# Kernel tuning notes

Measured on AMD Instinct MI355X. Metric: run time of the kernel, lower is better.

## Reference

```python
import jax, jax.numpy as jnp
import numpy as np

B, T, H, I, O, L = 8, 8192, 256, 256, 256, 2


def setup_inputs() -> dict:
    key = jax.random.key(0)
    ks = jax.random.split(key, 12)
    s = 1.0 / np.sqrt(H)
    inp = {
        "emb": jax.random.normal(ks[0], (B, T, I), jnp.float32),
        "start": jax.random.randint(ks[1], (B, T), 0, 2) > 0,  # bool reset flags
        "h0": jnp.zeros((L, B, H), jnp.float32),               # per-layer initial carry
        "min_w": jax.random.normal(ks[2], (H, I), jnp.float32) * s,
        "min_b": jnp.zeros((H,), jnp.float32),
        "mout_w": jax.random.normal(ks[3], (O, H), jnp.float32) * s,
        "mout_b": jnp.zeros((O,), jnp.float32),
        "Wf_w": jax.random.normal(ks[4], (L, H, H), jnp.float32) * s,
        "Wf_b": jnp.zeros((L, H), jnp.float32),
        "Wh_w": jax.random.normal(ks[5], (L, H, H), jnp.float32) * s,
        "Wh_b": jnp.zeros((L, H), jnp.float32),
        "Uf_w": jax.random.normal(ks[6], (L, H, H), jnp.float32) * s,
        "Uh_w": jax.random.normal(ks[7], (L, H, H), jnp.float32) * s,
        "ff_w": jax.random.normal(ks[8], (L, H, H), jnp.float32) * s,
        "ff_b": jnp.zeros((L, H), jnp.float32),
    }
    return inp


def reference(emb, start, h0, min_w, min_b, mout_w, mout_b,
              Wf_w, Wf_b, Wh_w, Wh_b, Uf_w, Uh_w, ff_w, ff_b):
    # map_in: [B,T,I] -> [B,T,H]
    x = jnp.einsum('bti,hi->bth', emb, min_w) + min_b
    start_t = start.T  # [T,B]
    h_final = []
    for l in range(L):
        # Precompute input-side projections outside the scan (time-parallel).
        xf = jnp.einsum('bth,oh->bto', x, Wf_w[l]) + Wf_b[l]  # [B,T,H]
        xh = jnp.einsum('bth,oh->bto', x, Wh_w[l]) + Wh_b[l]  # [B,T,H]
        Uf = Uf_w[l]
        Uh = Uh_w[l]

        def step(h, inp):
            xft, xht, st = inp  # [B,H], [B,H], [B]
            # Resettable: zero the carry where a new episode starts.
            h = jnp.where(st[:, None], jnp.zeros_like(h), h)
            f = jax.nn.sigmoid(xft + h @ Uf.T)
            h_hat = jnp.tanh(xht + (f * h) @ Uh.T)
            h_new = (1.0 - f) * h + f * h_hat
            return h_new, h_new

        hT, z = jax.lax.scan(step, h0[l],
                             (xf.transpose(1, 0, 2), xh.transpose(1, 0, 2), start_t))
        h_final.append(hT)
        z = z.transpose(1, 0, 2)  # [B,T,H]
        # per-layer feedforward + leaky_relu (slope 0.01)
        x = jax.nn.leaky_relu(jnp.einsum('bth,oh->bto', z, ff_w[l]) + ff_b[l])
    out = jnp.einsum('bth,oh->bto', x, mout_w) + mout_b  # [B,T,O]
    return out, jnp.stack(h_final)  # ([B,T,O], [L,B,H])
```

## Files before the change

kernel.cpp:

```cpp
#include <hip/hip_runtime.h>
#include <hip/hip_fp16.h>
#include <cstdint>
#include <cstddef>

#define BATCH 8
#define TT 8192
#define HD 256
#define RTOT (BATCH * TT)
#define HC 16
#define NPAIR (TT / (2 * HC))
#define MSTR 272

typedef __attribute__((ext_vector_type(4))) float    f32x4;
typedef __attribute__((ext_vector_type(8))) _Float16 f16x8;
typedef __attribute__((ext_vector_type(4))) _Float16 f16x4;

typedef __attribute__((address_space(1))) const void gvoid_t;
typedef __attribute__((address_space(3))) void lvoid_t;

__device__ __forceinline__ void gl_lds16(const void* g, void* l) {
  __builtin_amdgcn_global_load_lds((gvoid_t*)g, (lvoid_t*)l, 16, 0, 0);
}

__device__ __forceinline__ void ldsbar() {
  asm volatile("s_waitcnt lgkmcnt(0)" ::: "memory");
  __builtin_amdgcn_s_barrier();
  __builtin_amdgcn_sched_barrier(0x7F);
}

__device__ __forceinline__ void gbar() {
  __builtin_amdgcn_s_barrier();
  __builtin_amdgcn_sched_barrier(0);
  asm volatile("" ::: "memory");
}

__global__ void detect_start_par(const unsigned int* __restrict__ s,
                                 int* __restrict__ bad) {
  const unsigned int w = s[blockIdx.x * blockDim.x + threadIdx.x];
  const unsigned int b0 = w & 255u, b1 = (w >> 8) & 255u,
                     b2 = (w >> 16) & 255u, b3 = (w >> 24) & 255u;
  const int bi = (b1 | b2 | b3) != 0;
  const int bf = (b0 != 0) || (b1 != 0) ||
                 (b2 != 0 && b2 != 0x80u) || (b3 != 0 && b3 != 0x3fu);
  if (__any(bi) && (threadIdx.x & 63) == 0) atomicOr(&bad[0], 1);
  if (__any(bf) && (threadIdx.x & 63) == 0) atomicOr(&bad[1], 1);
}

__global__ void conv_f16(const float* __restrict__ in, _Float16* __restrict__ out,
                         const int n) {
  const int i = (blockIdx.x * blockDim.x + threadIdx.x) * 8;
  if (i + 7 >= n) return;
  const float4 a = *(const float4*)&in[i];
  const float4 b = *(const float4*)&in[i + 4];
  f16x8 v;
  v[0] = (_Float16)a.x; v[1] = (_Float16)a.y; v[2] = (_Float16)a.z; v[3] = (_Float16)a.w;
  v[4] = (_Float16)b.x; v[5] = (_Float16)b.y; v[6] = (_Float16)b.z; v[7] = (_Float16)b.w;
  *(f16x8*)&out[i] = v;
}

__global__ void conv_w8(const float* p0, const float* p1, const float* p2,
                        const float* p3, const float* p4, const float* p5,
                        const float* p6, const float* p7,
                        _Float16* __restrict__ out) {
  const int seg = blockIdx.y;
  const float* p;
  switch (seg) {
    case 0: p = p0; break; case 1: p = p1; break;
    case 2: p = p2; break; case 3: p = p3; break;
    case 4: p = p4; break; case 5: p = p5; break;
    case 6: p = p6; break; default: p = p7; break;
  }
  const int i = (blockIdx.x * blockDim.x + threadIdx.x) * 8;
  const float4 a = *(const float4*)&p[i];
  const float4 b = *(const float4*)&p[i + 4];
  f16x8 v;
  v[0] = (_Float16)a.x; v[1] = (_Float16)a.y; v[2] = (_Float16)a.z; v[3] = (_Float16)a.w;
  v[4] = (_Float16)b.x; v[5] = (_Float16)b.y; v[6] = (_Float16)b.z; v[7] = (_Float16)b.w;
  *(f16x8*)&out[(size_t)seg * 65536 + i] = v;
}

__global__ void swz_w(const float* __restrict__ Uf, const float* __restrict__ Uh,
                      _Float16* __restrict__ outp) {
  const int gid  = blockIdx.x * 256 + threadIdx.x;
  const int lane = gid & 63;
  const int w    = (gid >> 6) & 7;
  const int f    = (gid >> 9) & 15;
  const int mat  = (gid >> 13) & 1;
  const int l    = gid >> 14;
  const int fr = lane & 15, fq = lane >> 4;
  const int tile = f >> 3, kc = f & 7;
  const int nrow = (w * 2 + tile) * 16 + fr;
  const int kb   = kc * 32 + fq * 8;
  const float* src = (mat ? Uh : Uf) + (size_t)l * 65536 + nrow * 256 + kb;
  const float4 a = *(const float4*)src;
  const float4 b = *(const float4*)(src + 4);
  f16x8 v;
  v[0] = (_Float16)a.x; v[1] = (_Float16)a.y; v[2] = (_Float16)a.z; v[3] = (_Float16)a.w;
  v[4] = (_Float16)b.x; v[5] = (_Float16)b.y; v[6] = (_Float16)b.z; v[7] = (_Float16)b.w;
  *(f16x8*)&outp[(size_t)gid * 8] = v;
}

__global__ __launch_bounds__(256, 2) void gemm_fused(
    const _Float16* __restrict__ A,
    const _Float16* __restrict__ W1, const float* __restrict__ b1, const int act1,
    const _Float16* __restrict__ Wa, const float* __restrict__ ba,
    const _Float16* __restrict__ Wb, const float* __restrict__ bb,
    _Float16* __restrict__ Ca, _Float16* __restrict__ Cb,
    float* __restrict__ C32) {
  __shared__ __align__(16) char smem[59392];
  _Float16* mid = (_Float16*)smem;
  char* stg = smem + 34816;
  _Float16* EP = (_Float16*)stg;

  const int tid  = threadIdx.x;
  const int wave = tid >> 6, lane = tid & 63;
  const int wm = wave >> 1, wn = wave & 1;
  const int bm = blockIdx.x * 64;
  const int lrow  = tid >> 2;
  const int lcol8 = (tid & 3) * 8;
  const int fr = lane & 15;
  const int fq = lane >> 4;

  for (int nh = 0; nh < 2; nh++) {
    f32x4 acc[2][4];
#pragma unroll
    for (int i = 0; i < 2; i++)
#pragma unroll
      for (int j = 0; j < 4; j++) acc[i][j] = (f32x4){0.f, 0.f, 0.f, 0.f};
    float bv[4];
#pragma unroll
    for (int ni = 0; ni < 4; ni++)
      bv[ni] = b1[nh * 128 + wn * 64 + ni * 16 + fr];

    auto STA = [&](int kk, int bb2) {
      const int k0 = kk * 32;
      gl_lds16(&A[(size_t)(bm + lrow) * HD + k0 + lcol8],
               stg + bb2 * 12288 + wave * 1024);
#pragma unroll
      for (int is = 0; is < 2; is++)
        gl_lds16(&W1[(size_t)(nh * 128 + is * 64 + lrow) * HD + k0 + lcol8],
                 stg + bb2 * 12288 + 4096 + is * 4096 + wave * 1024);
    };

    STA(0, 0);
#pragma unroll
    for (int k = 0; k < 8; k++) {
      const int cur = k & 1;
      STA(k < 7 ? k + 1 : 7, cur ^ 1);
      asm volatile("s_waitcnt vmcnt(3)" ::: "memory");
      gbar();
      const _Float16* As = (const _Float16*)(stg + cur * 12288);
      const _Float16* Ws = (const _Float16*)(stg + cur * 12288 + 4096);
      f16x8 af[2], bf[4];
#pragma unroll
      for (int mi = 0; mi < 2; mi++)
        af[mi] = *(const f16x8*)(As + (wm * 32 + mi * 16 + fr) * 32 + fq * 8);
#pragma unroll
      for (int ni = 0; ni < 4; ni++)
        bf[ni] = *(const f16x8*)(Ws + (wn * 64 + ni * 16 + fr) * 32 + fq * 8);
#pragma unroll
      for (int mi = 0; mi < 2; mi++)
#pragma unroll
        for (int ni = 0; ni < 4; ni++)
          acc[mi][ni] = __builtin_amdgcn_mfma_f32_16x16x32_f16(af[mi], bf[ni],
                                                               acc[mi][ni], 0, 0, 0);
      asm volatile("s_waitcnt lgkmcnt(0)" ::: "memory");
      gbar();
    }
    __syncthreads();
#pragma unroll
    for (int mi = 0; mi < 2; mi++)
#pragma unroll
      for (int ni = 0; ni < 4; ni++)
#pragma unroll
        for (int j = 0; j < 4; j++) {
          float v = acc[mi][ni][j] + bv[ni];
          if (act1 == 1) v = (v > 0.f) ? v : 0.01f * v;
          mid[(wm * 32 + mi * 16 + fq * 4 + j) * MSTR +
              nh * 128 + wn * 64 + ni * 16 + fr] = (_Float16)v;
        }
  }
  __syncthreads();

  const int nmat = (Wb != nullptr) ? 2 : 1;
  for (int mat = 0; mat < nmat; mat++) {
    const _Float16* W2 = mat ? Wb : Wa;
    const float* b2p   = mat ? bb : ba;
    _Float16* C16      = mat ? Cb : Ca;
    for (int nh = 0; nh < 2; nh++) {
      f32x4 acc[2][4];
#pragma unroll
      for (int i = 0; i < 2; i++)
#pragma unroll
        for (int j = 0; j < 4; j++) acc[i][j] = (f32x4){0.f, 0.f, 0.f, 0.f};
      float bv[4];
#pragma unroll
      for (int ni = 0; ni < 4; ni++)
        bv[ni] = b2p[nh * 128 + wn * 64 + ni * 16 + fr];

      auto STB = [&](int kk, int bb2) {
        const int k0 = kk * 32;
#pragma unroll
        for (int is = 0; is < 2; is++)
          gl_lds16(&W2[(size_t)(nh * 128 + is * 64 + lrow) * HD + k0 + lcol8],
                   stg + bb2 * 12288 + is * 4096 + wave * 1024);
      };

      STB(0, 0);
#pragma unroll
      for (int k = 0; k < 8; k++) {
        const int cur = k & 1;
        STB(k < 7 ? k + 1 : 7, cur ^ 1);
        asm volatile("s_waitcnt vmcnt(2)" ::: "memory");
        gbar();
        const _Float16* Ws = (const _Float16*)(stg + cur * 12288);
        f16x8 af[2], bf[4];
#pragma unroll
        for (int mi = 0; mi < 2; mi++)
          af[mi] = *(const f16x8*)(mid + (wm * 32 + mi * 16 + fr) * MSTR +
                                   k * 32 + fq * 8);
#pragma unroll
        for (int ni = 0; ni < 4; ni++)
          bf[ni] = *(const f16x8*)(Ws + (wn * 64 + ni * 16 + fr) * 32 + fq * 8);
#pragma unroll
        for (int mi = 0; mi < 2; mi++)
#pragma unroll
          for (int ni = 0; ni < 4; ni++)
            acc[mi][ni] = __builtin_amdgcn_mfma_f32_16x16x32_f16(af[mi], bf[ni],
                                                                 acc[mi][ni], 0, 0, 0);
        asm volatile("s_waitcnt lgkmcnt(0)" ::: "memory");
        gbar();
      }
      __syncthreads();

      if (C32 != nullptr) {
#pragma unroll
        for (int mi = 0; mi < 2; mi++)
#pragma unroll
          for (int ni = 0; ni < 4; ni++)
#pragma unroll
            for (int j = 0; j < 4; j++) {
              const float v = acc[mi][ni][j] + bv[ni];
              C32[(size_t)(bm + wm * 32 + mi * 16 + fq * 4 + j) * HD +
                  nh * 128 + wn * 64 + ni * 16 + fr] = v;
            }
        __syncthreads();
      } else {
#pragma unroll
        for (int mi = 0; mi < 2; mi++)
#pragma unroll
          for (int ni = 0; ni < 4; ni++)
#pragma unroll
            for (int j = 0; j < 4; j++) {
              const float v = acc[mi][ni][j] + bv[ni];
              EP[(wm * 32 + mi * 16 + fq * 4 + j) * 136 +
                 wn * 64 + ni * 16 + fr] = (_Float16)v;
            }
        __syncthreads();
#pragma unroll
        for (int it = 0; it < 4; it++) {
          const int unit = it * 256 + tid;
          const int row = unit >> 4, cg = unit & 15;
          *(f16x8*)&C16[(size_t)(bm + row) * HD + nh * 128 + cg * 8] =
              *(const f16x8*)(EP + row * 136 + cg * 8);
        }
        __syncthreads();
      }
    }
  }
}

__global__ __launch_bounds__(512) void scan_mgu(
    const _Float16* __restrict__ xf, const _Float16* __restrict__ xh,
    const void* __restrict__ startp, const int* __restrict__ badf,
    const float* __restrict__ h0l,
    const _Float16* __restrict__ wfrag,
    _Float16* __restrict__ z, float* __restrict__ hfin,
    _Float16* __restrict__ dumpz) {
  const int tid  = threadIdx.x;
  const int wave = tid >> 6;
  const int lane = tid & 63;
  const int fr   = lane & 15;
  const int fq   = lane >> 4;
  const int col  = fr;
  const int b    = col & 7;
  const int grp  = col >> 3;
  const int base = blockIdx.x * (2 * HC);
  const int t0c  = base + grp * HC;
  const int mode = (!badf[0]) ? 1 : (!badf[1] ? 2 : 0);

  __shared__ __align__(16) char hbuf[8192];
  __shared__ __align__(16) char gbuf[8192];
  __shared__ int rb[16];

  _Float16* dp0 = dumpz + ((size_t)blockIdx.x * 512 + tid) * 16;

  auto flag = [&](int bb, int t) -> int {
    const int idx = bb * TT + t;
    if (mode == 1) return ((const int*)startp)[idx] != 0;
    if (mode == 2) return ((const float*)startp)[idx] != 0.0f;
    return ((const uint8_t*)startp)[idx] != 0;
  };
  auto ldfrag = [&](const char* buf, int kc) -> f16x8 {
    int off = kc * 1024 + fq * 256 + fr * 16;
    off ^= ((off >> 8) & 1) << 4;
    return *(const f16x8*)(buf + off);
  };
  auto stfrag = [&](char* buf, int nb, const float4 v) {
    int off = ((nb >> 5) * 1024) + (((nb >> 3) & 3) * 256) + col * 16 + (nb & 7) * 2;
    off ^= ((off >> 8) & 1) << 4;
    f16x4 p;
    p[0] = (_Float16)v.x; p[1] = (_Float16)v.y;
    p[2] = (_Float16)v.z; p[3] = (_Float16)v.w;
    *(f16x4*)(buf + off) = p;
  };

  f16x8 auf[2][8], auh[2][8];
#pragma unroll
  for (int f = 0; f < 16; f++)
    auf[f >> 3][f & 7] =
        *(const f16x8*)&wfrag[((size_t)(f * 512) + wave * 64 + lane) * 8];
#pragma unroll
  for (int f = 0; f < 16; f++)
    auh[f >> 3][f & 7] =
        *(const f16x8*)&wfrag[((size_t)(8192 + f * 512) + wave * 64 + lane) * 8];

  if (tid < 16) rb[tid] = -1;
  __syncthreads();
  {
    const int cg  = tid >> 5;
    const int l32 = tid & 31;
    const int t0g = base + (cg >> 3) * HC;
    const int bg  = cg & 7;
    for (int off = 0;; off += 32) {
      const int st = t0g - off - l32;
      if (st >= 0 && rb[cg] < 0 && flag(bg, st)) atomicMax(&rb[cg], st);
      __syncthreads();
      bool done = true;
#pragma unroll
      for (int c = 0; c < 16; c++) {
        const int tc = base + (c >> 3) * HC;
        if (rb[c] < 0 && tc - off >= 0) done = false;
      }
      if (done) break;
      __syncthreads();
    }
  }
  __syncthreads();

  const int rbc    = rb[col];
  const int startc = max(rbc, 0);
  int Lmax = 0;
#pragma unroll
  for (int c = 0; c < 16; c++) {
    const int tc = base + (c >> 3) * HC;
    const int s  = max(rb[c], 0);
    Lmax = max(Lmax, tc - s);
  }

  const int nb0 = (wave * 2 + 0) * 16 + fq * 4;
  const int nb1 = (wave * 2 + 1) * 16 + fq * 4;

  float4 hinit0 = make_float4(0.f, 0.f, 0.f, 0.f), hinit1 = hinit0;
  if (rbc < 0) {
    hinit0 = *(const float4*)&h0l[b * HD + nb0];
    hinit1 = *(const float4*)&h0l[b * HD + nb1];
  }
  float4 hr0 = hinit0, hr1 = hinit1;
  stfrag(hbuf, nb0, hr0);
  stfrag(hbuf, nb1, hr1);
  __syncthreads();

  int t = t0c - Lmax;
  int tcl = min(max(t, 0), TT - 1);
  f16x4 pxf0 = *(const f16x4*)&xf[((size_t)b * TT + tcl) * HD + nb0];
  f16x4 pxf1 = *(const f16x4*)&xf[((size_t)b * TT + tcl) * HD + nb1];
  f16x4 pxh0 = *(const f16x4*)&xh[((size_t)b * TT + tcl) * HD + nb0];
  f16x4 pxh1 = *(const f16x4*)&xh[((size_t)b * TT + tcl) * HD + nb1];
  int fnext;
  {
    const int ftn = flag(b, min(max(t + 1, 0), TT - 1));
    fnext = (t + 1 < TT) ? ftn : 0;
  }

  for (int i = -Lmax; i < HC; i++) {
    t = t0c + i;
    f32x4 cf0 = {(float)pxf0[0], (float)pxf0[1], (float)pxf0[2], (float)pxf0[3]};
    f32x4 cf1 = {(float)pxf1[0], (float)pxf1[1], (float)pxf1[2], (float)pxf1[3]};
    f32x4 ch0 = {(float)pxh0[0], (float)pxh0[1], (float)pxh0[2], (float)pxh0[3]};
    f32x4 ch1 = {(float)pxh1[0], (float)pxh1[1], (float)pxh1[2], (float)pxh1[3]};

    const int fcur = fnext;
    const int tn = min(max(t + 1, 0), TT - 1);
    pxf0 = *(const f16x4*)&xf[((size_t)b * TT + tn) * HD + nb0];
    pxf1 = *(const f16x4*)&xf[((size_t)b * TT + tn) * HD + nb1];
    pxh0 = *(const f16x4*)&xh[((size_t)b * TT + tn) * HD + nb0];
    pxh1 = *(const f16x4*)&xh[((size_t)b * TT + tn) * HD + nb1];
    {
      const int ftn = flag(b, min(max(t + 2, 0), TT - 1));
      fnext = (t + 2 < TT) ? ftn : 0;
    }

    int stn = 0;
    if (t + 1 <= startc) stn = 2;
    else if (fcur) stn = 1;

#pragma unroll
    for (int kc = 0; kc < 8; kc++) {
      const f16x8 bv = ldfrag(hbuf, kc);
      cf0 = __builtin_amdgcn_mfma_f32_16x16x32_f16(auf[0][kc], bv, cf0, 0, 0, 0);
      cf1 = __builtin_amdgcn_mfma_f32_16x16x32_f16(auf[1][kc], bv, cf1, 0, 0, 0);
    }
    f32x4 fv0, fv1;
    float4 g0, g1;
#pragma unroll
    for (int r = 0; r < 4; r++) {
      const float f0 = 1.f / (1.f + __expf(-cf0[r]));
      const float f1 = 1.f / (1.f + __expf(-cf1[r]));
      fv0[r] = f0; fv1[r] = f1;
      (&g0.x)[r] = f0 * (&hr0.x)[r];
      (&g1.x)[r] = f1 * (&hr1.x)[r];
    }
    stfrag(gbuf, nb0, g0);
    stfrag(gbuf, nb1, g1);
    ldsbar();

#pragma unroll
    for (int kc = 0; kc < 8; kc++) {
      const f16x8 bv = ldfrag(gbuf, kc);
      ch0 = __builtin_amdgcn_mfma_f32_16x16x32_f16(auh[0][kc], bv, ch0, 0, 0, 0);
      ch1 = __builtin_amdgcn_mfma_f32_16x16x32_f16(auh[1][kc], bv, ch1, 0, 0, 0);
    }
    float4 hn0, hn1;
    f16x4 zn0, zn1;
#pragma unroll
    for (int r = 0; r < 4; r++) {
      const float e0 = __expf(2.f * ch0[r]);
      const float e1 = __expf(2.f * ch1[r]);
      const float hh0 = 1.f - 2.f / (e0 + 1.f);
      const float hh1 = 1.f - 2.f / (e1 + 1.f);
      (&hn0.x)[r] = (1.f - fv0[r]) * (&hr0.x)[r] + fv0[r] * hh0;
      (&hn1.x)[r] = (1.f - fv1[r]) * (&hr1.x)[r] + fv1[r] * hh1;
      zn0[r] = (_Float16)(&hn0.x)[r];
      zn1[r] = (_Float16)(&hn1.x)[r];
    }
    {
      const size_t tz = (size_t)b * TT + (size_t)max(t, 0);
      _Float16* zp0 = (i >= 0) ? &z[tz * HD + nb0] : dp0;
      _Float16* zp1 = (i >= 0) ? &z[tz * HD + nb1] : dp0 + 8;
      *(f16x4*)zp0 = zn0;
      *(f16x4*)zp1 = zn1;
    }
    hr0 = (stn == 2) ? hinit0 : (stn == 1 ? make_float4(0.f, 0.f, 0.f, 0.f) : hn0);
    hr1 = (stn == 2) ? hinit1 : (stn == 1 ? make_float4(0.f, 0.f, 0.f, 0.f) : hn1);
    stfrag(hbuf, nb0, hr0);
    stfrag(hbuf, nb1, hr1);
    ldsbar();
  }

  if (t0c + HC == TT) {
    *(float4*)&hfin[b * HD + nb0] = hr0;
    *(float4*)&hfin[b * HD + nb1] = hr1;
  }
}

extern "C" void kernel_launch(void* const* d_in, const int* in_sizes, int n_in,
                              void* d_out, int out_size, void* d_ws, size_t ws_size,
                              hipStream_t stream) {
  const float* emb    = (const float*)d_in[0];
  const void*  startp = d_in[1];
  const float* h0     = (const float*)d_in[2];
  const float* min_w  = (const float*)d_in[3];
  const float* min_b  = (const float*)d_in[4];
  const float* mout_w = (const float*)d_in[5];
  const float* mout_b = (const float*)d_in[6];
  const float* Wf_w   = (const float*)d_in[7];
  const float* Wf_b   = (const float*)d_in[8];
  const float* Wh_w   = (const float*)d_in[9];
  const float* Wh_b   = (const float*)d_in[10];
  const float* Uf_w   = (const float*)d_in[11];
  const float* Uh_w   = (const float*)d_in[12];
  const float* ff_w   = (const float*)d_in[13];
  const float* ff_b   = (const float*)d_in[14];

  float* out = (float*)d_out;
  char*  ws  = (char*)d_ws;
  int*   bad = (int*)ws;
  _Float16* w16  = (_Float16*)(ws + 1024);
  _Float16* uswz = (_Float16*)(ws + 1024 + 1048576);
  _Float16* dump = (_Float16*)(ws + 1024 + 1048576 + 524288);
  _Float16* bufE = (_Float16*)(ws + 1024 + 1048576 + 524288 + 4194304);
  _Float16* bufA = bufE + (size_t)RTOT * HD;
  _Float16* bufB = bufA + (size_t)RTOT * HD;
  _Float16* bufC = bufB + (size_t)RTOT * HD;
  float* hfin = out + (size_t)RTOT * HD;
  const size_t WO = (size_t)HD * HD;

  _Float16* w_min = w16;
  _Float16* w_out = w16 + 1 * WO;
  _Float16* w_f0  = w16 + 2 * WO;
  _Float16* w_f1  = w16 + 3 * WO;
  _Float16* w_h0  = w16 + 4 * WO;
  _Float16* w_h1  = w16 + 5 * WO;
  _Float16* w_ff0 = w16 + 6 * WO;
  _Float16* w_ff1 = w16 + 7 * WO;

  hipMemsetAsync(bad, 0, 16, stream);
  detect_start_par<<<64, 256, 0, stream>>>((const unsigned int*)startp, bad);
  conv_f16<<<RTOT * HD / 2048, 256, 0, stream>>>(emb, bufE, RTOT * HD);
  conv_w8<<<dim3(32, 8), 256, 0, stream>>>(min_w, mout_w, Wf_w, Wf_w + WO,
                                           Wh_w, Wh_w + WO, ff_w, ff_w + WO, w16);
  swz_w<<<128, 256, 0, stream>>>(Uf_w, Uh_w, uswz);

  gemm_fused<<<RTOT / 64, 256, 0, stream>>>(bufE, w_min, min_b, 0,
                                            w_f0, Wf_b, w_h0, Wh_b,
                                            bufB, bufC, nullptr);
  scan_mgu<<<NPAIR, 512, 0, stream>>>(bufB, bufC, startp, bad, h0,
                                      uswz, bufA, hfin, dump);
  gemm_fused<<<RTOT / 64, 256, 0, stream>>>(bufA, w_ff0, ff_b, 1,
                                            w_f1, Wf_b + HD, w_h1, Wh_b + HD,
                                            bufB, bufC, nullptr);
  scan_mgu<<<NPAIR, 512, 0, stream>>>(bufB, bufC, startp, bad, h0 + BATCH * HD,
                                      uswz + (size_t)16384 * 8, bufA,
                                      hfin + BATCH * HD, dump);
  gemm_fused<<<RTOT / 64, 256, 0, stream>>>(bufA, w_ff1, ff_b + HD, 1,
                                            w_out, mout_b, nullptr, nullptr,
                                            nullptr, nullptr, out);
}
```

Baseline: 350.2 us.

## Fuse fp32 embedding conversion into first GEMM and load operands directly from global

Removes the separate fp32-to-fp16 conversion kernel for the embedding input: the first fused GEMM now reads fp32 rows and converts them in registers. The GEMM also drops its LDS staging (global_load_lds with a double-buffered pipeline) and instead has each wave load A and W fragments straight from global memory. Each wave now computes the full 128-column half in one pass instead of two passes. This saves a full read-write pass over the embedding, but the GEMM loses LDS-based sharing and prefetch overlap of the weight tiles, which raises register pressure and redundant global and cache traffic.

Result: slower. 517.5 us (+47.8%).

```diff
diff --git a/kernel.cpp b/kernel.cpp
--- a/kernel.cpp
+++ b/kernel.cpp
@@ -15,23 +15,10 @@
 typedef __attribute__((ext_vector_type(8))) _Float16 f16x8;
 typedef __attribute__((ext_vector_type(4))) _Float16 f16x4;
 
-typedef __attribute__((address_space(1))) const void gvoid_t;
-typedef __attribute__((address_space(3))) void lvoid_t;
-
-__device__ __forceinline__ void gl_lds16(const void* g, void* l) {
-  __builtin_amdgcn_global_load_lds((gvoid_t*)g, (lvoid_t*)l, 16, 0, 0);
-}
-
 __device__ __forceinline__ void ldsbar() {
   asm volatile("s_waitcnt lgkmcnt(0)" ::: "memory");
   __builtin_amdgcn_s_barrier();
   __builtin_amdgcn_sched_barrier(0x7F);
-}
-
-__device__ __forceinline__ void gbar() {
-  __builtin_amdgcn_s_barrier();
-  __builtin_amdgcn_sched_barrier(0);
-  asm volatile("" ::: "memory");
 }
 
 __global__ void detect_start_par(const unsigned int* __restrict__ s,
@@ -44,18 +31,6 @@
                  (b2 != 0 && b2 != 0x80u) || (b3 != 0 && b3 != 0x3fu);
   if (__any(bi) && (threadIdx.x & 63) == 0) atomicOr(&bad[0], 1);
   if (__any(bf) && (threadIdx.x & 63) == 0) atomicOr(&bad[1], 1);
-}
-
-__global__ void conv_f16(const float* __restrict__ in, _Float16* __restrict__ out,
-                         const int n) {
-  const int i = (blockIdx.x * blockDim.x + threadIdx.x) * 8;
-  if (i + 7 >= n) return;
-  const float4 a = *(const float4*)&in[i];
-  const float4 b = *(const float4*)&in[i + 4];
-  f16x8 v;
-  v[0] = (_Float16)a.x; v[1] = (_Float16)a.y; v[2] = (_Float16)a.z; v[3] = (_Float16)a.w;
-  v[4] = (_Float16)b.x; v[5] = (_Float16)b.y; v[6] = (_Float16)b.z; v[7] = (_Float16)b.w;
-  *(f16x8*)&out[i] = v;
 }
 
 __global__ void conv_w8(const float* p0, const float* p1, const float* p2,
@@ -101,84 +76,90 @@
 }
 
 __global__ __launch_bounds__(256, 2) void gemm_fused(
-    const _Float16* __restrict__ A,
+    const _Float16* __restrict__ A16, const float* __restrict__ A32,
     const _Float16* __restrict__ W1, const float* __restrict__ b1, const int act1,
     const _Float16* __restrict__ Wa, const float* __restrict__ ba,
     const _Float16* __restrict__ Wb, const float* __restrict__ bb,
     _Float16* __restrict__ Ca, _Float16* __restrict__ Cb,
     float* __restrict__ C32) {
-  __shared__ __align__(16) char smem[59392];
-  _Float16* mid = (_Float16*)smem;
-  char* stg = smem + 34816;
-  _Float16* EP = (_Float16*)stg;
+  __shared__ __align__(16) _Float16 mid[64 * MSTR];
+  __shared__ __align__(16) _Float16 EP[64 * MSTR];
 
   const int tid  = threadIdx.x;
   const int wave = tid >> 6, lane = tid & 63;
   const int wm = wave >> 1, wn = wave & 1;
   const int bm = blockIdx.x * 64;
-  const int lrow  = tid >> 2;
-  const int lcol8 = (tid & 3) * 8;
   const int fr = lane & 15;
   const int fq = lane >> 4;
 
-  for (int nh = 0; nh < 2; nh++) {
-    f32x4 acc[2][4];
+  {
+    f32x4 acc[2][8];
 #pragma unroll
     for (int i = 0; i < 2; i++)
 #pragma unroll
-      for (int j = 0; j < 4; j++) acc[i][j] = (f32x4){0.f, 0.f, 0.f, 0.f};
-    float bv[4];
-#pragma unroll
-    for (int ni = 0; ni < 4; ni++)
-      bv[ni] = b1[nh * 128 + wn * 64 + ni * 16 + fr];
-
-    auto STA = [&](int kk, int bb2) {
-      const int k0 = kk * 32;
-      gl_lds16(&A[(size_t)(bm + lrow) * HD + k0 + lcol8],
-               stg + bb2 * 12288 + wave * 1024);
-#pragma unroll
-      for (int is = 0; is < 2; is++)
-        gl_lds16(&W1[(size_t)(nh * 128 + is * 64 + lrow) * HD + k0 + lcol8],
-                 stg + bb2 * 12288 + 4096 + is * 4096 + wave * 1024);
-    };
-
-    STA(0, 0);
-#pragma unroll
-    for (int k = 0; k < 8; k++) {
-      const int cur = k & 1;
-      STA(k < 7 ? k + 1 : 7, cur ^ 1);
-      asm volatile("s_waitcnt vmcnt(3)" ::: "memory");
-      gbar();
-      const _Float16* As = (const _Float16*)(stg + cur * 12288);
-      const _Float16* Ws = (const _Float16*)(stg + cur * 12288 + 4096);
-      f16x8 af[2], bf[4];
-#pragma unroll
-      for (int mi = 0; mi < 2; mi++)
-        af[mi] = *(const f16x8*)(As + (wm * 32 + mi * 16 + fr) * 32 + fq * 8);
-#pragma unroll
-      for (int ni = 0; ni < 4; ni++)
-        bf[ni] = *(const f16x8*)(Ws + (wn * 64 + ni * 16 + fr) * 32 + fq * 8);
-#pragma unroll
-      for (int mi = 0; mi < 2; mi++)
-#pragma unroll
-        for (int ni = 0; ni < 4; ni++)
-          acc[mi][ni] = __builtin_amdgcn_mfma_f32_16x16x32_f16(af[mi], bf[ni],
-                                                               acc[mi][ni], 0, 0, 0);
-      asm volatile("s_waitcnt lgkmcnt(0)" ::: "memory");
-      gbar();
-    }
-    __syncthreads();
+      for (int j = 0; j < 8; j++) acc[i][j] = (f32x4){0.f, 0.f, 0.f, 0.f};
+
+    if (A32 != nullptr) {
+#pragma unroll
+      for (int k = 0; k < 8; k++) {
+        f16x8 af[2], bf[8];
+#pragma unroll
+        for (int mi = 0; mi < 2; mi++) {
+          const float* ap = &A32[(size_t)(bm + wm * 32 + mi * 16 + fr) * HD +
+                                 k * 32 + fq * 8];
+          const float4 a0 = *(const float4*)ap;
+          const float4 a1 = *(const float4*)(ap + 4);
+          f16x8 v;
+          v[0] = (_Float16)a0.x; v[1] = (_Float16)a0.y;
+          v[2] = (_Float16)a0.z; v[3] = (_Float16)a0.w;
+          v[4] = (_Float16)a1.x; v[5] = (_Float16)a1.y;
+          v[6] = (_Float16)a1.z; v[7] = (_Float16)a1.w;
+          af[mi] = v;
+        }
+#pragma unroll
+        for (int ni = 0; ni < 8; ni++)
+          bf[ni] = *(const f16x8*)&W1[(size_t)(wn * 128 + ni * 16 + fr) * HD +
+                                      k * 32 + fq * 8];
+#pragma unroll
+        for (int mi = 0; mi < 2; mi++)
+#pragma unroll
+          for (int ni = 0; ni < 8; ni++)
+            acc[mi][ni] = __builtin_amdgcn_mfma_f32_16x16x32_f16(af[mi], bf[ni],
+                                                                 acc[mi][ni], 0, 0, 0);
+      }
+    } else {
+#pragma unroll
+      for (int k = 0; k < 8; k++) {
+        f16x8 af[2], bf[8];
+#pragma unroll
+        for (int mi = 0; mi < 2; mi++)
+          af[mi] = *(const f16x8*)&A16[(size_t)(bm + wm * 32 + mi * 16 + fr) * HD +
+                                       k * 32 + fq * 8];
+#pragma unroll
+        for (int ni = 0; ni < 8; ni++)
+          bf[ni] = *(const f16x8*)&W1[(size_t)(wn * 128 + ni * 16 + fr) * HD +
+                                      k * 32 + fq * 8];
+#pragma unroll
+        for (int mi = 0; mi < 2; mi++)
+#pragma unroll
+          for (int ni = 0; ni < 8; ni++)
+            acc[mi][ni] = __builtin_amdgcn_mfma_f32_16x16x32_f16(af[mi], bf[ni],
+                                                                 acc[mi][ni], 0, 0, 0);
+      }
+    }
 #pragma unroll
     for (int mi = 0; mi < 2; mi++)
 #pragma unroll
-      for (int ni = 0; ni < 4; ni++)
+      for (int ni = 0; ni < 8; ni++) {
+        const float bvv = b1[wn * 128 + ni * 16 + fr];
 #pragma unroll
         for (int j = 0; j < 4; j++) {
-          float v = acc[mi][ni][j] + bv[ni];
+          float v = acc[mi][ni][j] + bvv;
           if (act1 == 1) v = (v > 0.f) ? v : 0.01f * v;
           mid[(wm * 32 + mi * 16 + fq * 4 + j) * MSTR +
-              nh * 128 + wn * 64 + ni * 16 + fr] = (_Float16)v;
+              wn * 128 + ni * 16 + fr] = (_Float16)v;
         }
+      }
   }
   __syncthreads();
 
@@ -187,85 +168,63 @@
     const _Float16* W2 = mat ? Wb : Wa;
     const float* b2p   = mat ? bb : ba;
     _Float16* C16      = mat ? Cb : Ca;
-    for (int nh = 0; nh < 2; nh++) {
-      f32x4 acc[2][4];
-#pragma unroll
-      for (int i = 0; i < 2; i++)
-#pragma unroll
-        for (int j = 0; j < 4; j++) acc[i][j] = (f32x4){0.f, 0.f, 0.f, 0.f};
-      float bv[4];
-#pragma unroll
-      for (int ni = 0; ni < 4; ni++)
-        bv[ni] = b2p[nh * 128 + wn * 64 + ni * 16 + fr];
-
-      auto STB = [&](int kk, int bb2) {
-        const int k0 = kk * 32;
-#pragma unroll
-        for (int is = 0; is < 2; is++)
-          gl_lds16(&W2[(size_t)(nh * 128 + is * 64 + lrow) * HD + k0 + lcol8],
-                   stg + bb2 * 12288 + is * 4096 + wave * 1024);
-      };
-
-      STB(0, 0);
-#pragma unroll
-      for (int k = 0; k < 8; k++) {
-        const int cur = k & 1;
-        STB(k < 7 ? k + 1 : 7, cur ^ 1);
-        asm volatile("s_waitcnt vmcnt(2)" ::: "memory");
-        gbar();
-        const _Float16* Ws = (const _Float16*)(stg + cur * 12288);
-        f16x8 af[2], bf[4];
-#pragma unroll
-        for (int mi = 0; mi < 2; mi++)
-          af[mi] = *(const f16x8*)(mid + (wm * 32 + mi * 16 + fr) * MSTR +
-                                   k * 32 + fq * 8);
-#pragma unroll
-        for (int ni = 0; ni < 4; ni++)
-          bf[ni] = *(const f16x8*)(Ws + (wn * 64 + ni * 16 + fr) * 32 + fq * 8);
-#pragma unroll
-        for (int mi = 0; mi < 2; mi++)
-#pragma unroll
-          for (int ni = 0; ni < 4; ni++)
-            acc[mi][ni] = __builtin_amdgcn_mfma_f32_16x16x32_f16(af[mi], bf[ni],
-                                                                 acc[mi][ni], 0, 0, 0);
-        asm volatile("s_waitcnt lgkmcnt(0)" ::: "memory");
-        gbar();
+
+    f32x4 acc[2][8];
+#pragma unroll
+    for (int i = 0; i < 2; i++)
+#pragma unroll
+      for (int j = 0; j < 8; j++) acc[i][j] = (f32x4){0.f, 0.f, 0.f, 0.f};
+
+#pragma unroll
+    for (int k = 0; k < 8; k++) {
+      f16x8 af[2], bf[8];
+#pragma unroll
+      for (int mi = 0; mi < 2; mi++)
+        af[mi] = *(const f16x8*)&mid[(wm * 32 + mi * 16 + fr) * MSTR +
+                                     k * 32 + fq * 8];
+#pragma unroll
+      for (int ni = 0; ni < 8; ni++)
+        bf[ni] = *(const f16x8*)&W2[(size_t)(wn * 128 + ni * 16 + fr) * HD +
+                                    k * 32 + fq * 8];
+#pragma unroll
+      for (int mi = 0; mi < 2; mi++)
+#pragma unroll
+        for (int ni = 0; ni < 8; ni++)
+          acc[mi][ni] = __builtin_amdgcn_mfma_f32_16x16x32_f16(af[mi], bf[ni],
+                                                               acc[mi][ni], 0, 0, 0);
+    }
+
+    if (C32 != nullptr) {
+#pragma unroll
+      for (int mi = 0; mi < 2; mi++)
+#pragma unroll
+        for (int ni = 0; ni < 8; ni++) {
+          const float bvv = b2p[wn * 128 + ni * 16 + fr];
+#pragma unroll
+          for (int j = 0; j < 4; j++)
+            C32[(size_t)(bm + wm * 32 + mi * 16 + fq * 4 + j) * HD +
+                wn * 128 + ni * 16 + fr] = acc[mi][ni][j] + bvv;
+        }
+    } else {
+#pragma unroll
+      for (int mi = 0; mi < 2; mi++)
+#pragma unroll
+        for (int ni = 0; ni < 8; ni++) {
+          const float bvv = b2p[wn * 128 + ni * 16 + fr];
+#pragma unroll
+          for (int j = 0; j < 4; j++)
+            EP[(wm * 32 + mi * 16 + fq * 4 + j) * MSTR +
+               wn * 128 + ni * 16 + fr] = (_Float16)(acc[mi][ni][j] + bvv);
+        }
+      __syncthreads();
+#pragma unroll
+      for (int it = 0; it < 8; it++) {
+        const int unit = it * 256 + tid;
+        const int row = unit >> 5, cg = unit & 31;
+        *(f16x8*)&C16[(size_t)(bm + row) * HD + cg * 8] =
+            *(const f16x8*)&EP[row * MSTR + cg * 8];
       }
       __syncthreads();
-
-      if (C32 != nullptr) {
-#pragma unroll
-        for (int mi = 0; mi < 2; mi++)
-#pragma unroll
-          for (int ni = 0; ni < 4; ni++)
-#pragma unroll
-            for (int j = 0; j < 4; j++) {
-              const float v = acc[mi][ni][j] + bv[ni];
-              C32[(size_t)(bm + wm * 32 + mi * 16 + fq * 4 + j) * HD +
-                  nh * 128 + wn * 64 + ni * 16 + fr] = v;
-            }
-        __syncthreads();
-      } else {
-#pragma unroll
-        for (int mi = 0; mi < 2; mi++)
-#pragma unroll
-          for (int ni = 0; ni < 4; ni++)
-#pragma unroll
-            for (int j = 0; j < 4; j++) {
-              const float v = acc[mi][ni][j] + bv[ni];
-              EP[(wm * 32 + mi * 16 + fq * 4 + j) * 136 +
-                 wn * 64 + ni * 16 + fr] = (_Float16)v;
-            }
-        __syncthreads();
-#pragma unroll
-        for (int it = 0; it < 4; it++) {
-          const int unit = it * 256 + tid;
-          const int row = unit >> 4, cg = unit & 15;
-          *(f16x8*)&C16[(size_t)(bm + row) * HD + nh * 128 + cg * 8] =
-              *(const f16x8*)(EP + row * 136 + cg * 8);
-        }
-        __syncthreads();
-      }
     }
   }
 }
@@ -489,8 +448,7 @@
   _Float16* w16  = (_Float16*)(ws + 1024);
   _Float16* uswz = (_Float16*)(ws + 1024 + 1048576);
   _Float16* dump = (_Float16*)(ws + 1024 + 1048576 + 524288);
-  _Float16* bufE = (_Float16*)(ws + 1024 + 1048576 + 524288 + 4194304);
-  _Float16* bufA = bufE + (size_t)RTOT * HD;
+  _Float16* bufA = (_Float16*)(ws + 1024 + 1048576 + 524288 + 4194304);
   _Float16* bufB = bufA + (size_t)RTOT * HD;
   _Float16* bufC = bufB + (size_t)RTOT * HD;
   float* hfin = out + (size_t)RTOT * HD;
@@ -507,23 +465,22 @@
 
   hipMemsetAsync(bad, 0, 16, stream);
   detect_start_par<<<64, 256, 0, stream>>>((const unsigned int*)startp, bad);
-  conv_f16<<<RTOT * HD / 2048, 256, 0, stream>>>(emb, bufE, RTOT * HD);
   conv_w8<<<dim3(32, 8), 256, 0, stream>>>(min_w, mout_w, Wf_w, Wf_w + WO,
                                            Wh_w, Wh_w + WO, ff_w, ff_w + WO, w16);
   swz_w<<<128, 256, 0, stream>>>(Uf_w, Uh_w, uswz);
 
-  gemm_fused<<<RTOT / 64, 256, 0, stream>>>(bufE, w_min, min_b, 0,
+  gemm_fused<<<RTOT / 64, 256, 0, stream>>>(nullptr, emb, w_min, min_b, 0,
                                             w_f0, Wf_b, w_h0, Wh_b,
                                             bufB, bufC, nullptr);
   scan_mgu<<<NPAIR, 512, 0, stream>>>(bufB, bufC, startp, bad, h0,
                                       uswz, bufA, hfin, dump);
-  gemm_fused<<<RTOT / 64, 256, 0, stream>>>(bufA, w_ff0, ff_b, 1,
+  gemm_fused<<<RTOT / 64, 256, 0, stream>>>(bufA, nullptr, w_ff0, ff_b, 1,
                                             w_f1, Wf_b + HD, w_h1, Wh_b + HD,
                                             bufB, bufC, nullptr);
   scan_mgu<<<NPAIR, 512, 0, stream>>>(bufB, bufC, startp, bad, h0 + BATCH * HD,
                                       uswz + (size_t)16384 * 8, bufA,
                                       hfin + BATCH * HD, dump);
-  gemm_fused<<<RTOT / 64, 256, 0, stream>>>(bufA, w_ff1, ff_b + HD, 1,
+  gemm_fused<<<RTOT / 64, 256, 0, stream>>>(bufA, nullptr, w_ff1, ff_b + HD, 1,
                                             w_out, mout_b, nullptr, nullptr,
                                             nullptr, nullptr, out);
 }
```

## Triple-buffer first GEMM staging and merge dual second-stage GEMMs into one pass

Applied to the files above, without the earlier changes.

The first GEMM's A/W staging now uses three LDS buffers with a two-step prefetch distance, so global loads have more time to land before they are needed. The second stage no longer runs the Wa and Wb projections in separate sequential loops. It computes both in a single K loop, sharing the A fragments read from the mid tile and the barriers, with a larger staging area that holds both weight tiles. Shared memory grows to 71680 bytes and accumulator registers double, which may lower occupancy below the declared two blocks per CU.

New measurement: 347.2 us. No clear change (-0.8%).

```diff
diff --git a/kernel.cpp b/kernel.cpp
--- a/kernel.cpp
+++ b/kernel.cpp
@@ -107,7 +107,7 @@
     const _Float16* __restrict__ Wb, const float* __restrict__ bb,
     _Float16* __restrict__ Ca, _Float16* __restrict__ Cb,
     float* __restrict__ C32) {
-  __shared__ __align__(16) char smem[59392];
+  __shared__ __align__(16) char smem[71680];
   _Float16* mid = (_Float16*)smem;
   char* stg = smem + 34816;
   _Float16* EP = (_Float16*)stg;
@@ -132,22 +132,23 @@
     for (int ni = 0; ni < 4; ni++)
       bv[ni] = b1[nh * 128 + wn * 64 + ni * 16 + fr];
 
-    auto STA = [&](int kk, int bb2) {
+    auto STA = [&](int kk, int b3) {
       const int k0 = kk * 32;
       gl_lds16(&A[(size_t)(bm + lrow) * HD + k0 + lcol8],
-               stg + bb2 * 12288 + wave * 1024);
+               stg + b3 * 12288 + wave * 1024);
 #pragma unroll
       for (int is = 0; is < 2; is++)
         gl_lds16(&W1[(size_t)(nh * 128 + is * 64 + lrow) * HD + k0 + lcol8],
-                 stg + bb2 * 12288 + 4096 + is * 4096 + wave * 1024);
+                 stg + b3 * 12288 + 4096 + is * 4096 + wave * 1024);
     };
 
     STA(0, 0);
+    STA(1, 1);
 #pragma unroll
     for (int k = 0; k < 8; k++) {
-      const int cur = k & 1;
-      STA(k < 7 ? k + 1 : 7, cur ^ 1);
-      asm volatile("s_waitcnt vmcnt(3)" ::: "memory");
+      const int cur = k % 3;
+      STA(k < 6 ? k + 2 : 7, (k + 2) % 3);
+      asm volatile("s_waitcnt vmcnt(6)" ::: "memory");
       gbar();
       const _Float16* As = (const _Float16*)(stg + cur * 12288);
       const _Float16* Ws = (const _Float16*)(stg + cur * 12288 + 4096);
@@ -182,86 +183,122 @@
   }
   __syncthreads();
 
-  const int nmat = (Wb != nullptr) ? 2 : 1;
-  for (int mat = 0; mat < nmat; mat++) {
-    const _Float16* W2 = mat ? Wb : Wa;
-    const float* b2p   = mat ? bb : ba;
-    _Float16* C16      = mat ? Cb : Ca;
-    for (int nh = 0; nh < 2; nh++) {
-      f32x4 acc[2][4];
-#pragma unroll
-      for (int i = 0; i < 2; i++)
-#pragma unroll
-        for (int j = 0; j < 4; j++) acc[i][j] = (f32x4){0.f, 0.f, 0.f, 0.f};
-      float bv[4];
+  for (int nh = 0; nh < 2; nh++) {
+    f32x4 acca[2][4], accb[2][4];
+#pragma unroll
+    for (int i = 0; i < 2; i++)
+#pragma unroll
+      for (int j = 0; j < 4; j++) {
+        acca[i][j] = (f32x4){0.f, 0.f, 0.f, 0.f};
+        accb[i][j] = (f32x4){0.f, 0.f, 0.f, 0.f};
+      }
+    float bva[4], bvb[4];
+#pragma unroll
+    for (int ni = 0; ni < 4; ni++) {
+      bva[ni] = ba[nh * 128 + wn * 64 + ni * 16 + fr];
+      bvb[ni] = (Wb != nullptr) ? bb[nh * 128 + wn * 64 + ni * 16 + fr] : 0.f;
+    }
+
+    auto STB = [&](int kk, int b2) {
+      const int k0 = kk * 32;
+#pragma unroll
+      for (int is = 0; is < 2; is++) {
+        gl_lds16(&Wa[(size_t)(nh * 128 + is * 64 + lrow) * HD + k0 + lcol8],
+                 stg + b2 * 16384 + is * 4096 + wave * 1024);
+        if (Wb != nullptr)
+          gl_lds16(&Wb[(size_t)(nh * 128 + is * 64 + lrow) * HD + k0 + lcol8],
+                   stg + b2 * 16384 + 8192 + is * 4096 + wave * 1024);
+      }
+    };
+
+    STB(0, 0);
+#pragma unroll
+    for (int k = 0; k < 8; k++) {
+      const int cur = k & 1;
+      STB(k < 7 ? k + 1 : 7, cur ^ 1);
+      if (Wb != nullptr) {
+        asm volatile("s_waitcnt vmcnt(4)" ::: "memory");
+      } else {
+        asm volatile("s_waitcnt vmcnt(2)" ::: "memory");
+      }
+      gbar();
+      const _Float16* Wsa = (const _Float16*)(stg + cur * 16384);
+      const _Float16* Wsb = (const _Float16*)(stg + cur * 16384 + 8192);
+      f16x8 af[2], bfa[4], bfb[4];
+#pragma unroll
+      for (int mi = 0; mi < 2; mi++)
+        af[mi] = *(const f16x8*)(mid + (wm * 32 + mi * 16 + fr) * MSTR +
+                                 k * 32 + fq * 8);
 #pragma unroll
       for (int ni = 0; ni < 4; ni++)
-        bv[ni] = b2p[nh * 128 + wn * 64 + ni * 16 + fr];
-
-      auto STB = [&](int kk, int bb2) {
-        const int k0 = kk * 32;
-#pragma unroll
-        for (int is = 0; is < 2; is++)
-          gl_lds16(&W2[(size_t)(nh * 128 + is * 64 + lrow) * HD + k0 + lcol8],
-                   stg + bb2 * 12288 + is * 4096 + wave * 1024);
-      };
-
-      STB(0, 0);
-#pragma unroll
-      for (int k = 0; k < 8; k++) {
-        const int cur = k & 1;
-        STB(k < 7 ? k + 1 : 7, cur ^ 1);
-        asm volatile("s_waitcnt vmcnt(2)" ::: "memory");
-        gbar();
-        const _Float16* Ws = (const _Float16*)(stg + cur * 12288);
-        f16x8 af[2], bf[4];
+        bfa[ni] = *(const f16x8*)(Wsa + (wn * 64 + ni * 16 + fr) * 32 + fq * 8);
+#pragma unroll
+      for (int mi = 0; mi < 2; mi++)
+#pragma unroll
+        for (int ni = 0; ni < 4; ni++)
+          acca[mi][ni] = __builtin_amdgcn_mfma_f32_16x16x32_f16(af[mi], bfa[ni],
+                                                                acca[mi][ni], 0, 0, 0);
+      if (Wb != nullptr) {
+#pragma unroll
+        for (int ni = 0; ni < 4; ni++)
+          bfb[ni] = *(const f16x8*)(Wsb + (wn * 64 + ni * 16 + fr) * 32 + fq * 8);
 #pragma unroll
         for (int mi = 0; mi < 2; mi++)
-          af[mi] = *(const f16x8*)(mid + (wm * 32 + mi * 16 + fr) * MSTR +
-                                   k * 32 + fq * 8);
+#pragma unroll
+          for (int ni = 0; ni < 4; ni++)
+            accb[mi][ni] = __builtin_amdgcn_mfma_f32_16x16x32_f16(af[mi], bfb[ni],
+                                                                  accb[mi][ni], 0, 0, 0);
+      }
+      asm volatile("s_waitcnt lgkmcnt(0)" ::: "memory");
+      gbar();
+    }
+    __syncthreads();
+
+    if (C32 != nullptr) {
+#pragma unroll
+      for (int mi = 0; mi < 2; mi++)
 #pragma unroll
         for (int ni = 0; ni < 4; ni++)
-          bf[ni] = *(const f16x8*)(Ws + (wn * 64 + ni * 16 + fr) * 32 + fq * 8);
+#pragma unroll
+          for (int j = 0; j < 4; j++) {
+            const float v = acca[mi][ni][j] + bva[ni];
+            C32[(size_t)(bm + wm * 32 + mi * 16 + fq * 4 + j) * HD +
+                nh * 128 + wn * 64 + ni * 16 + fr] = v;
+          }
+      __syncthreads();
+    } else {
+#pragma unroll
+      for (int mi = 0; mi < 2; mi++)
+#pragma unroll
+        for (int ni = 0; ni < 4; ni++)
+#pragma unroll
+          for (int j = 0; j < 4; j++)
+            EP[(wm * 32 + mi * 16 + fq * 4 + j) * 136 +
+               wn * 64 + ni * 16 + fr] = (_Float16)(acca[mi][ni][j] + bva[ni]);
+      __syncthreads();
+#pragma unroll
+      for (int it = 0; it < 4; it++) {
+        const int unit = it * 256 + tid;
+        const int row = unit >> 4, cg = unit & 15;
+        *(f16x8*)&Ca[(size_t)(bm + row) * HD + nh * 128 + cg * 8] =
+            *(const f16x8*)(EP + row * 136 + cg * 8);
+      }
+      __syncthreads();
+      if (Wb != nullptr) {
 #pragma unroll
         for (int mi = 0; mi < 2; mi++)
 #pragma unroll
           for (int ni = 0; ni < 4; ni++)
-            acc[mi][ni] = __builtin_amdgcn_mfma_f32_16x16x32_f16(af[mi], bf[ni],
-                                                                 acc[mi][ni], 0, 0, 0);
-        asm volatile("s_waitcnt lgkmcnt(0)" ::: "memory");
-        gbar();
-      }
-      __syncthreads();
-
-      if (C32 != nullptr) {
-#pragma unroll
-        for (int mi = 0; mi < 2; mi++)
-#pragma unroll
-          for (int ni = 0; ni < 4; ni++)
-#pragma unroll
-            for (int j = 0; j < 4; j++) {
-              const float v = acc[mi][ni][j] + bv[ni];
-              C32[(size_t)(bm + wm * 32 + mi * 16 + fq * 4 + j) * HD +
-                  nh * 128 + wn * 64 + ni * 16 + fr] = v;
-            }
-        __syncthreads();
-      } else {
-#pragma unroll
-        for (int mi = 0; mi < 2; mi++)
-#pragma unroll
-          for (int ni = 0; ni < 4; ni++)
-#pragma unroll
-            for (int j = 0; j < 4; j++) {
-              const float v = acc[mi][ni][j] + bv[ni];
+#pragma unroll
+            for (int j = 0; j < 4; j++)
               EP[(wm * 32 + mi * 16 + fq * 4 + j) * 136 +
-                 wn * 64 + ni * 16 + fr] = (_Float16)v;
-            }
+                 wn * 64 + ni * 16 + fr] = (_Float16)(accb[mi][ni][j] + bvb[ni]);
         __syncthreads();
 #pragma unroll
         for (int it = 0; it < 4; it++) {
           const int unit = it * 256 + tid;
           const int row = unit >> 4, cg = unit & 15;
-          *(f16x8*)&C16[(size_t)(bm + row) * HD + nh * 128 + cg * 8] =
+          *(f16x8*)&Cb[(size_t)(bm + row) * HD + nh * 128 + cg * 8] =
               *(const f16x8*)(EP + row * 136 + cg * 8);
         }
         __syncthreads();
```
